# Performance work log

Hardware: AMD Instinct MI355X
Metric: run time of the kernel (lower is better)

Reference implementation:

```python
import jax, jax.numpy as jnp
import numpy as np


def setup_inputs() -> dict:
    key = jax.random.key(0)
    ks = jax.random.split(key, 12)
    B = 131072
    s = lambda fan_in: 1.0 / np.sqrt(fan_in)
    inp = {
        "x": jax.random.normal(ks[0], (B, 2, 13, 21), dtype=jnp.float32),
        # depthwise 3x3, groups=2, no bias: OIHW with O=2, I=1
        "dw_w": jax.random.uniform(ks[1], (2, 1, 3, 3), jnp.float32, -s(9), s(9)),
        # pointwise 1x1: 2 -> 5
        "pw_w": jax.random.uniform(ks[2], (5, 2, 1, 1), jnp.float32, -s(2), s(2)),
        "pw_b": jax.random.uniform(ks[3], (5,), jnp.float32, -s(2), s(2)),
        # conv 1x1: 5 -> 5
        "conv_w": jax.random.uniform(ks[4], (5, 5, 1, 1), jnp.float32, -s(5), s(5)),
        "conv_b": jax.random.uniform(ks[5], (5,), jnp.float32, -s(5), s(5)),
        # dense 90 -> 16 -> 16 -> 14 (torch Linear layout: [out, in])
        "w1": jax.random.uniform(ks[6], (16, 90), jnp.float32, -s(90), s(90)),
        "b1": jax.random.uniform(ks[7], (16,), jnp.float32, -s(90), s(90)),
        "w2": jax.random.uniform(ks[8], (16, 16), jnp.float32, -s(16), s(16)),
        "b2": jax.random.uniform(ks[9], (16,), jnp.float32, -s(16), s(16)),
        "w3": jax.random.uniform(ks[10], (14, 16), jnp.float32, -s(16), s(16)),
        "b3": jax.random.uniform(ks[11], (14,), jnp.float32, -s(16), s(16)),
    }
    return inp


def _conv(x, w, groups=1):
    return jax.lax.conv_general_dilated(
        x, w, window_strides=(1, 1), padding="VALID",
        dimension_numbers=("NCHW", "OIHW", "NCHW"),
        feature_group_count=groups)


def reference(x, dw_w, pw_w, pw_b, conv_w, conv_b, w1, b1, w2, b2, w3, b3):
    # depthwise-separable conv: depthwise 3x3 (groups=2, no bias) + pointwise 1x1
    h = _conv(x, dw_w, groups=2)                      # [B,2,11,19]
    h = _conv(h, pw_w) + pw_b[None, :, None, None]    # [B,5,11,19]
    h = jnp.tanh(h)
    h = _conv(h, conv_w) + conv_b[None, :, None, None]  # 1x1 conv 5->5
    h = jnp.tanh(h)
    # AvgPool2d(3): kernel=stride=3, no padding -> crop to 9x18, reshape-mean
    h = h[:, :, :9, :18]
    B = h.shape[0]
    h = h.reshape(B, 5, 3, 3, 6, 3).mean(axis=(3, 5))  # [B,5,3,6]
    h = jnp.tanh(h)
    h = h.reshape(B, 90)
    h = jnp.tanh(h @ w1.T + b1)
    h = jnp.tanh(h @ w2.T + b2)
    return h @ w3.T + b3                               # [B,14]
```

## Files before the change

### kernel.cpp

```cpp
#include <hip/hip_runtime.h>

typedef float f4v __attribute__((ext_vector_type(4), aligned(4)));
typedef float f2v __attribute__((ext_vector_type(2), aligned(4)));

__device__ __forceinline__ float fast_tanh(float x) {
  float t = x * 2.8853900817779268f;
  float e = __builtin_amdgcn_exp2f(t);
  float r = __builtin_amdgcn_rcpf(e + 1.0f);
  return 1.0f - 2.0f * r;
}

__global__ __launch_bounds__(256, 3) void smartpixel_kernel(
    const float* __restrict__ x, const float* __restrict__ dww,
    const float* __restrict__ pww, const float* __restrict__ pwb,
    const float* __restrict__ cvw, const float* __restrict__ cvb,
    const float* __restrict__ w1, const float* __restrict__ b1,
    const float* __restrict__ w2, const float* __restrict__ b2,
    const float* __restrict__ w3, const float* __restrict__ b3,
    float* __restrict__ out, int nsamp) {
  const int g = blockIdx.x * 256 + threadIdx.x;
  const int s = g >> 1;
  const int t = g & 1;
  if (s >= nsamp) return;
  const float* xb = x + (long)s * 546 + t * 9;

  float A0[12], A1[12], A2[12], A3[12];
  float B0[12], B1[12], B2[12], B3[12];

#define LDROW(S, R)                                                        \
  do {                                                                     \
    _Pragma("unroll") for (int kk = 0; kk < 3; ++kk) {                     \
      f4v va = *reinterpret_cast<const f4v*>(xb + (R) * 21 + 4 * kk);      \
      f4v vb = *reinterpret_cast<const f4v*>(xb + 273 + (R) * 21 + 4 * kk);\
      _Pragma("unroll") for (int l = 0; l < 4; ++l) {                      \
        A##S[4 * kk + l] = va[l];                                          \
        B##S[4 * kk + l] = vb[l];                                          \
      }                                                                    \
    }                                                                      \
  } while (0)

  float pool[5][3];
#pragma unroll
  for (int c = 0; c < 5; ++c)
#pragma unroll
    for (int pc = 0; pc < 3; ++pc) pool[c][pc] = 0.0f;

  float h1a[16];
#pragma unroll
  for (int o = 0; o < 16; ++o) h1a[o] = (t == 0) ? b1[o] : 0.0f;

  const float* w1t = w1 + 3 * t;

#define ROWBODY(SA, SB, SC)                                                   \
  do {                                                                        \
    _Pragma("unroll") for (int j = 0; j < 9; ++j) {                           \
      float d0 = A##SA[j] * dww[0] + A##SA[j + 1] * dww[1] + A##SA[j + 2] * dww[2]  \
               + A##SB[j] * dww[3] + A##SB[j + 1] * dww[4] + A##SB[j + 2] * dww[5]  \
               + A##SC[j] * dww[6] + A##SC[j + 1] * dww[7] + A##SC[j + 2] * dww[8]; \
      float d1 = B##SA[j] * dww[9]  + B##SA[j + 1] * dww[10] + B##SA[j + 2] * dww[11] \
               + B##SB[j] * dww[12] + B##SB[j + 1] * dww[13] + B##SB[j + 2] * dww[14] \
               + B##SC[j] * dww[15] + B##SC[j + 1] * dww[16] + B##SC[j + 2] * dww[17];\
      float aa0 = fast_tanh(pwb[0] + pww[0] * d0 + pww[1] * d1);              \
      float aa1 = fast_tanh(pwb[1] + pww[2] * d0 + pww[3] * d1);              \
      float aa2 = fast_tanh(pwb[2] + pww[4] * d0 + pww[5] * d1);              \
      float aa3 = fast_tanh(pwb[3] + pww[6] * d0 + pww[7] * d1);              \
      float aa4 = fast_tanh(pwb[4] + pww[8] * d0 + pww[9] * d1);              \
      _Pragma("unroll") for (int q = 0; q < 5; ++q) {                         \
        float acc = cvb[q] + cvw[5 * q] * aa0 + cvw[5 * q + 1] * aa1          \
                  + cvw[5 * q + 2] * aa2 + cvw[5 * q + 3] * aa3               \
                  + cvw[5 * q + 4] * aa4;                                     \
        pool[q][j / 3] += fast_tanh(acc);                                     \
      }                                                                       \
    }                                                                         \
  } while (0)

#define POOLFIN(RR)                                                           \
  do {                                                                        \
    _Pragma("unroll") for (int c = 0; c < 5; ++c) {                           \
      _Pragma("unroll") for (int pc = 0; pc < 3; ++pc) {                      \
        float pv = fast_tanh(pool[c][pc] * (1.0f / 9.0f));                    \
        pool[c][pc] = 0.0f;                                                   \
        _Pragma("unroll") for (int o = 0; o < 16; ++o) {                      \
          h1a[o] += pv * w1t[o * 90 + c * 18 + (RR) * 6 + pc];                \
        }                                                                     \
      }                                                                       \
    }                                                                         \
  } while (0)

  LDROW(0, 0); LDROW(1, 1); LDROW(2, 2);
  LDROW(3, 3);  ROWBODY(0, 1, 2);
  LDROW(0, 4);  ROWBODY(1, 2, 3);
  LDROW(1, 5);  ROWBODY(2, 3, 0); POOLFIN(0);
  LDROW(2, 6);  ROWBODY(3, 0, 1);
  LDROW(3, 7);  ROWBODY(0, 1, 2);
  LDROW(0, 8);  ROWBODY(1, 2, 3); POOLFIN(1);
  LDROW(1, 9);  ROWBODY(2, 3, 0);
  LDROW(2, 10); ROWBODY(3, 0, 1);
                ROWBODY(0, 1, 2); POOLFIN(2);

#pragma unroll
  for (int o = 0; o < 16; ++o) h1a[o] += __shfl_xor(h1a[o], 1, 64);

  float h1[16];
#pragma unroll
  for (int k = 0; k < 16; ++k) h1[k] = fast_tanh(h1a[k]);

  float h2[16];
#pragma unroll
  for (int o = 0; o < 16; ++o) {
    float acc = b2[o];
#pragma unroll
    for (int k = 0; k < 16; ++k) acc += h1[k] * w2[o * 16 + k];
    h2[o] = fast_tanh(acc);
  }

  const int ob = 7 * t;
  float ov[7];
#pragma unroll
  for (int oo = 0; oo < 7; ++oo) {
    float acc = b3[ob + oo];
#pragma unroll
    for (int k = 0; k < 16; ++k) acc += h2[k] * w3[(ob + oo) * 16 + k];
    ov[oo] = acc;
  }
  float* po = out + (long)s * 14 + ob;
  f4v v4; v4[0] = ov[0]; v4[1] = ov[1]; v4[2] = ov[2]; v4[3] = ov[3];
  *reinterpret_cast<f4v*>(po) = v4;
  f2v v2; v2[0] = ov[4]; v2[1] = ov[5];
  *reinterpret_cast<f2v*>(po + 4) = v2;
  po[6] = ov[6];
}

extern "C" void kernel_launch(void* const* d_in, const int* in_sizes, int n_in,
                              void* d_out, int out_size, void* d_ws, size_t ws_size,
                              hipStream_t stream) {
  const float* x      = (const float*)d_in[0];
  const float* dw_w   = (const float*)d_in[1];
  const float* pw_w   = (const float*)d_in[2];
  const float* pw_b   = (const float*)d_in[3];
  const float* conv_w = (const float*)d_in[4];
  const float* conv_b = (const float*)d_in[5];
  const float* w1     = (const float*)d_in[6];
  const float* b1     = (const float*)d_in[7];
  const float* w2     = (const float*)d_in[8];
  const float* b2     = (const float*)d_in[9];
  const float* w3     = (const float*)d_in[10];
  const float* b3     = (const float*)d_in[11];
  float* out = (float*)d_out;

  int nsamp = in_sizes[0] / 546;
  long nthreads = 2L * nsamp;
  int blocks = (int)((nthreads + 255) / 256);
  smartpixel_kernel<<<blocks, 256, 0, stream>>>(
      x, dw_w, pw_w, pw_b, conv_w, conv_b, w1, b1, w2, b2, w3, b3, out, nsamp);
}
```

Measured before the change: 127.3 us.

## Roll row pipeline into a two-iteration loop and hoist weights into scalars

Replaces the fully unrolled 11-row sweep with a two-iteration non-unrolled loop that keeps the 4-slot rolling row buffers, and hoists all conv weights into named scalar constants loaded once. Converts arrays to explicit scalars, vectorizes w1/w3 weight loads, splits the b1 bias as half per thread, and changes launch bounds to a waves-per-eu range of 2–3. The aim is smaller code size and less instruction-cache pressure with controlled register use. The cost is a loop back-edge, predicated pool-finish branches, and possibly lower occupancy if the compiler settles on 2 waves.

```diff
diff --git a/kernel.cpp b/kernel.cpp
--- a/kernel.cpp
+++ b/kernel.cpp
@@ -10,7 +10,9 @@
   return 1.0f - 2.0f * r;
 }
 
-__global__ __launch_bounds__(256, 3) void smartpixel_kernel(
+__global__ __launch_bounds__(256)
+__attribute__((amdgpu_waves_per_eu(2, 3)))
+void smartpixel_kernel(
     const float* __restrict__ x, const float* __restrict__ dww,
     const float* __restrict__ pww, const float* __restrict__ pwb,
     const float* __restrict__ cvw, const float* __restrict__ cvb,
@@ -24,111 +26,163 @@
   if (s >= nsamp) return;
   const float* xb = x + (long)s * 546 + t * 9;
 
-  float A0[12], A1[12], A2[12], A3[12];
-  float B0[12], B1[12], B2[12], B3[12];
-
-#define LDROW(S, R)                                                        \
-  do {                                                                     \
-    _Pragma("unroll") for (int kk = 0; kk < 3; ++kk) {                     \
-      f4v va = *reinterpret_cast<const f4v*>(xb + (R) * 21 + 4 * kk);      \
-      f4v vb = *reinterpret_cast<const f4v*>(xb + 273 + (R) * 21 + 4 * kk);\
-      _Pragma("unroll") for (int l = 0; l < 4; ++l) {                      \
-        A##S[4 * kk + l] = va[l];                                          \
-        B##S[4 * kk + l] = vb[l];                                          \
-      }                                                                    \
-    }                                                                      \
+  const float kd0 = dww[0], kd1 = dww[1], kd2 = dww[2], kd3 = dww[3], kd4 = dww[4],
+              kd5 = dww[5], kd6 = dww[6], kd7 = dww[7], kd8 = dww[8], kd9 = dww[9],
+              kd10 = dww[10], kd11 = dww[11], kd12 = dww[12], kd13 = dww[13],
+              kd14 = dww[14], kd15 = dww[15], kd16 = dww[16], kd17 = dww[17];
+  const float kp0 = pww[0], kp1 = pww[1], kp2 = pww[2], kp3 = pww[3], kp4 = pww[4],
+              kp5 = pww[5], kp6 = pww[6], kp7 = pww[7], kp8 = pww[8], kp9 = pww[9];
+  const float kb0 = pwb[0], kb1 = pwb[1], kb2 = pwb[2], kb3 = pwb[3], kb4 = pwb[4];
+  const float kc0 = cvw[0], kc1 = cvw[1], kc2 = cvw[2], kc3 = cvw[3], kc4 = cvw[4],
+              kc5 = cvw[5], kc6 = cvw[6], kc7 = cvw[7], kc8 = cvw[8], kc9 = cvw[9],
+              kc10 = cvw[10], kc11 = cvw[11], kc12 = cvw[12], kc13 = cvw[13],
+              kc14 = cvw[14], kc15 = cvw[15], kc16 = cvw[16], kc17 = cvw[17],
+              kc18 = cvw[18], kc19 = cvw[19], kc20 = cvw[20], kc21 = cvw[21],
+              kc22 = cvw[22], kc23 = cvw[23], kc24 = cvw[24];
+  const float kcb0 = cvb[0], kcb1 = cvb[1], kcb2 = cvb[2], kcb3 = cvb[3], kcb4 = cvb[4];
+
+#define DECLROW(P) float P##_0, P##_1, P##_2, P##_3, P##_4, P##_5, P##_6, P##_7, P##_8, P##_9, P##_10, P##_11;
+  DECLROW(A0) DECLROW(A1) DECLROW(A2) DECLROW(A3)
+  DECLROW(B0) DECLROW(B1) DECLROW(B2) DECLROW(B3)
+
+#define LDROW(S, BASE, R)                                                   \
+  do {                                                                      \
+    f4v va0 = *reinterpret_cast<const f4v*>((BASE) + (R) * 21 + 0);         \
+    f4v va1 = *reinterpret_cast<const f4v*>((BASE) + (R) * 21 + 4);         \
+    f4v va2 = *reinterpret_cast<const f4v*>((BASE) + (R) * 21 + 8);         \
+    f4v vb0 = *reinterpret_cast<const f4v*>((BASE) + 273 + (R) * 21 + 0);   \
+    f4v vb1 = *reinterpret_cast<const f4v*>((BASE) + 273 + (R) * 21 + 4);   \
+    f4v vb2 = *reinterpret_cast<const f4v*>((BASE) + 273 + (R) * 21 + 8);   \
+    A##S##_0 = va0[0]; A##S##_1 = va0[1]; A##S##_2 = va0[2]; A##S##_3 = va0[3]; \
+    A##S##_4 = va1[0]; A##S##_5 = va1[1]; A##S##_6 = va1[2]; A##S##_7 = va1[3]; \
+    A##S##_8 = va2[0]; A##S##_9 = va2[1]; A##S##_10 = va2[2]; A##S##_11 = va2[3]; \
+    B##S##_0 = vb0[0]; B##S##_1 = vb0[1]; B##S##_2 = vb0[2]; B##S##_3 = vb0[3]; \
+    B##S##_4 = vb1[0]; B##S##_5 = vb1[1]; B##S##_6 = vb1[2]; B##S##_7 = vb1[3]; \
+    B##S##_8 = vb2[0]; B##S##_9 = vb2[1]; B##S##_10 = vb2[2]; B##S##_11 = vb2[3]; \
   } while (0)
 
-  float pool[5][3];
-#pragma unroll
-  for (int c = 0; c < 5; ++c)
-#pragma unroll
-    for (int pc = 0; pc < 3; ++pc) pool[c][pc] = 0.0f;
-
-  float h1a[16];
-#pragma unroll
-  for (int o = 0; o < 16; ++o) h1a[o] = (t == 0) ? b1[o] : 0.0f;
+  float P0_0 = 0.f, P0_1 = 0.f, P0_2 = 0.f;
+  float P1_0 = 0.f, P1_1 = 0.f, P1_2 = 0.f;
+  float P2_0 = 0.f, P2_1 = 0.f, P2_2 = 0.f;
+  float P3_0 = 0.f, P3_1 = 0.f, P3_2 = 0.f;
+  float P4_0 = 0.f, P4_1 = 0.f, P4_2 = 0.f;
+  float H0 = 0.5f * b1[0], H1 = 0.5f * b1[1], H2 = 0.5f * b1[2], H3 = 0.5f * b1[3],
+        H4 = 0.5f * b1[4], H5 = 0.5f * b1[5], H6 = 0.5f * b1[6], H7 = 0.5f * b1[7],
+        H8 = 0.5f * b1[8], H9 = 0.5f * b1[9], H10 = 0.5f * b1[10], H11 = 0.5f * b1[11],
+        H12 = 0.5f * b1[12], H13 = 0.5f * b1[13], H14 = 0.5f * b1[14], H15 = 0.5f * b1[15];
+
+#define POS(SA, SB, SC, J0, J1, J2, G)                                        \
+  do {                                                                        \
+    float d0 = A##SA##_##J0 * kd0 + A##SA##_##J1 * kd1 + A##SA##_##J2 * kd2   \
+             + A##SB##_##J0 * kd3 + A##SB##_##J1 * kd4 + A##SB##_##J2 * kd5   \
+             + A##SC##_##J0 * kd6 + A##SC##_##J1 * kd7 + A##SC##_##J2 * kd8;  \
+    float d1 = B##SA##_##J0 * kd9 + B##SA##_##J1 * kd10 + B##SA##_##J2 * kd11 \
+             + B##SB##_##J0 * kd12 + B##SB##_##J1 * kd13 + B##SB##_##J2 * kd14\
+             + B##SC##_##J0 * kd15 + B##SC##_##J1 * kd16 + B##SC##_##J2 * kd17;\
+    float u0 = fast_tanh(kb0 + kp0 * d0 + kp1 * d1);                          \
+    float u1 = fast_tanh(kb1 + kp2 * d0 + kp3 * d1);                          \
+    float u2 = fast_tanh(kb2 + kp4 * d0 + kp5 * d1);                          \
+    float u3 = fast_tanh(kb3 + kp6 * d0 + kp7 * d1);                          \
+    float u4 = fast_tanh(kb4 + kp8 * d0 + kp9 * d1);                          \
+    P0_##G += fast_tanh(kcb0 + kc0 * u0 + kc1 * u1 + kc2 * u2 + kc3 * u3 + kc4 * u4);   \
+    P1_##G += fast_tanh(kcb1 + kc5 * u0 + kc6 * u1 + kc7 * u2 + kc8 * u3 + kc9 * u4);   \
+    P2_##G += fast_tanh(kcb2 + kc10 * u0 + kc11 * u1 + kc12 * u2 + kc13 * u3 + kc14 * u4); \
+    P3_##G += fast_tanh(kcb3 + kc15 * u0 + kc16 * u1 + kc17 * u2 + kc18 * u3 + kc19 * u4); \
+    P4_##G += fast_tanh(kcb4 + kc20 * u0 + kc21 * u1 + kc22 * u2 + kc23 * u3 + kc24 * u4); \
+  } while (0)
+
+#define ROWBODY(SA, SB, SC)                                                   \
+  POS(SA, SB, SC, 0, 1, 2, 0); POS(SA, SB, SC, 1, 2, 3, 0);                   \
+  POS(SA, SB, SC, 2, 3, 4, 0); POS(SA, SB, SC, 3, 4, 5, 1);                   \
+  POS(SA, SB, SC, 4, 5, 6, 1); POS(SA, SB, SC, 5, 6, 7, 1);                   \
+  POS(SA, SB, SC, 6, 7, 8, 2); POS(SA, SB, SC, 7, 8, 9, 2);                   \
+  POS(SA, SB, SC, 8, 9, 10, 2);
 
   const float* w1t = w1 + 3 * t;
 
-#define ROWBODY(SA, SB, SC)                                                   \
+#define ACC1(O, WP, p0_, p1_, p2_)                                            \
+  {                                                                           \
+    f2v wv = *reinterpret_cast<const f2v*>((WP) + (O) * 90);                  \
+    float ws = (WP)[(O) * 90 + 2];                                            \
+    H##O += p0_ * wv[0] + p1_ * wv[1] + p2_ * ws;                             \
+  }
+
+#define FCH(C, RR)                                                            \
   do {                                                                        \
-    _Pragma("unroll") for (int j = 0; j < 9; ++j) {                           \
-      float d0 = A##SA[j] * dww[0] + A##SA[j + 1] * dww[1] + A##SA[j + 2] * dww[2]  \
-               + A##SB[j] * dww[3] + A##SB[j + 1] * dww[4] + A##SB[j + 2] * dww[5]  \
-               + A##SC[j] * dww[6] + A##SC[j + 1] * dww[7] + A##SC[j + 2] * dww[8]; \
-      float d1 = B##SA[j] * dww[9]  + B##SA[j + 1] * dww[10] + B##SA[j + 2] * dww[11] \
-               + B##SB[j] * dww[12] + B##SB[j + 1] * dww[13] + B##SB[j + 2] * dww[14] \
-               + B##SC[j] * dww[15] + B##SC[j + 1] * dww[16] + B##SC[j + 2] * dww[17];\
-      float aa0 = fast_tanh(pwb[0] + pww[0] * d0 + pww[1] * d1);              \
-      float aa1 = fast_tanh(pwb[1] + pww[2] * d0 + pww[3] * d1);              \
-      float aa2 = fast_tanh(pwb[2] + pww[4] * d0 + pww[5] * d1);              \
-      float aa3 = fast_tanh(pwb[3] + pww[6] * d0 + pww[7] * d1);              \
-      float aa4 = fast_tanh(pwb[4] + pww[8] * d0 + pww[9] * d1);              \
-      _Pragma("unroll") for (int q = 0; q < 5; ++q) {                         \
-        float acc = cvb[q] + cvw[5 * q] * aa0 + cvw[5 * q + 1] * aa1          \
-                  + cvw[5 * q + 2] * aa2 + cvw[5 * q + 3] * aa3               \
-                  + cvw[5 * q + 4] * aa4;                                     \
-        pool[q][j / 3] += fast_tanh(acc);                                     \
-      }                                                                       \
-    }                                                                         \
+    float pv0 = fast_tanh(P##C##_0 * (1.0f / 9.0f)); P##C##_0 = 0.f;          \
+    float pv1 = fast_tanh(P##C##_1 * (1.0f / 9.0f)); P##C##_1 = 0.f;          \
+    float pv2 = fast_tanh(P##C##_2 * (1.0f / 9.0f)); P##C##_2 = 0.f;          \
+    const float* wp_ = w1t + (C) * 18 + (RR) * 6;                             \
+    ACC1(0, wp_, pv0, pv1, pv2) ACC1(1, wp_, pv0, pv1, pv2)                   \
+    ACC1(2, wp_, pv0, pv1, pv2) ACC1(3, wp_, pv0, pv1, pv2)                   \
+    ACC1(4, wp_, pv0, pv1, pv2) ACC1(5, wp_, pv0, pv1, pv2)                   \
+    ACC1(6, wp_, pv0, pv1, pv2) ACC1(7, wp_, pv0, pv1, pv2)                   \
+    ACC1(8, wp_, pv0, pv1, pv2) ACC1(9, wp_, pv0, pv1, pv2)                   \
+    ACC1(10, wp_, pv0, pv1, pv2) ACC1(11, wp_, pv0, pv1, pv2)                 \
+    ACC1(12, wp_, pv0, pv1, pv2) ACC1(13, wp_, pv0, pv1, pv2)                 \
+    ACC1(14, wp_, pv0, pv1, pv2) ACC1(15, wp_, pv0, pv1, pv2)                 \
   } while (0)
 
-#define POOLFIN(RR)                                                           \
-  do {                                                                        \
-    _Pragma("unroll") for (int c = 0; c < 5; ++c) {                           \
-      _Pragma("unroll") for (int pc = 0; pc < 3; ++pc) {                      \
-        float pv = fast_tanh(pool[c][pc] * (1.0f / 9.0f));                    \
-        pool[c][pc] = 0.0f;                                                   \
-        _Pragma("unroll") for (int o = 0; o < 16; ++o) {                      \
-          h1a[o] += pv * w1t[o * 90 + c * 18 + (RR) * 6 + pc];                \
-        }                                                                     \
-      }                                                                       \
-    }                                                                         \
-  } while (0)
-
-  LDROW(0, 0); LDROW(1, 1); LDROW(2, 2);
-  LDROW(3, 3);  ROWBODY(0, 1, 2);
-  LDROW(0, 4);  ROWBODY(1, 2, 3);
-  LDROW(1, 5);  ROWBODY(2, 3, 0); POOLFIN(0);
-  LDROW(2, 6);  ROWBODY(3, 0, 1);
-  LDROW(3, 7);  ROWBODY(0, 1, 2);
-  LDROW(0, 8);  ROWBODY(1, 2, 3); POOLFIN(1);
-  LDROW(1, 9);  ROWBODY(2, 3, 0);
-  LDROW(2, 10); ROWBODY(3, 0, 1);
-                ROWBODY(0, 1, 2); POOLFIN(2);
-
-#pragma unroll
-  for (int o = 0; o < 16; ++o) h1a[o] += __shfl_xor(h1a[o], 1, 64);
-
-  float h1[16];
-#pragma unroll
-  for (int k = 0; k < 16; ++k) h1[k] = fast_tanh(h1a[k]);
-
-  float h2[16];
-#pragma unroll
-  for (int o = 0; o < 16; ++o) {
-    float acc = b2[o];
-#pragma unroll
-    for (int k = 0; k < 16; ++k) acc += h1[k] * w2[o * 16 + k];
-    h2[o] = fast_tanh(acc);
+#define POOLFIN(RR) FCH(0, RR); FCH(1, RR); FCH(2, RR); FCH(3, RR); FCH(4, RR);
+
+  LDROW(0, xb, 0); LDROW(1, xb, 1); LDROW(2, xb, 2);
+
+#pragma unroll 1
+  for (int ig = 0; ig < 2; ++ig) {
+    const float* xr = xb + (long)ig * 84;
+    LDROW(3, xr, 3);
+    ROWBODY(0, 1, 2);
+    LDROW(0, xr, 4);
+    ROWBODY(1, 2, 3);
+    if (ig == 1) { POOLFIN(1); }
+    LDROW(1, xr, 5);
+    ROWBODY(2, 3, 0);
+    if (ig == 0) { POOLFIN(0); }
+    LDROW(2, xr, 6);
+    ROWBODY(3, 0, 1);
   }
+  ROWBODY(0, 1, 2);
+  POOLFIN(2);
+
+#define COMB(O) H##O += __shfl_xor(H##O, 1, 64); H##O = fast_tanh(H##O);
+  COMB(0) COMB(1) COMB(2) COMB(3) COMB(4) COMB(5) COMB(6) COMB(7)
+  COMB(8) COMB(9) COMB(10) COMB(11) COMB(12) COMB(13) COMB(14) COMB(15)
+
+#define FC2(O)                                                                \
+  float q##O = fast_tanh(b2[(O)]                                              \
+      + H0 * w2[(O) * 16 + 0] + H1 * w2[(O) * 16 + 1] + H2 * w2[(O) * 16 + 2] \
+      + H3 * w2[(O) * 16 + 3] + H4 * w2[(O) * 16 + 4] + H5 * w2[(O) * 16 + 5] \
+      + H6 * w2[(O) * 16 + 6] + H7 * w2[(O) * 16 + 7] + H8 * w2[(O) * 16 + 8] \
+      + H9 * w2[(O) * 16 + 9] + H10 * w2[(O) * 16 + 10]                       \
+      + H11 * w2[(O) * 16 + 11] + H12 * w2[(O) * 16 + 12]                     \
+      + H13 * w2[(O) * 16 + 13] + H14 * w2[(O) * 16 + 14]                     \
+      + H15 * w2[(O) * 16 + 15]);
+  FC2(0) FC2(1) FC2(2) FC2(3) FC2(4) FC2(5) FC2(6) FC2(7)
+  FC2(8) FC2(9) FC2(10) FC2(11) FC2(12) FC2(13) FC2(14) FC2(15)
 
   const int ob = 7 * t;
-  float ov[7];
-#pragma unroll
-  for (int oo = 0; oo < 7; ++oo) {
-    float acc = b3[ob + oo];
-#pragma unroll
-    for (int k = 0; k < 16; ++k) acc += h2[k] * w3[(ob + oo) * 16 + k];
-    ov[oo] = acc;
+  const float* w3t = w3 + ob * 16;
+#define OUT1(OO)                                                              \
+  float o##OO;                                                                \
+  {                                                                           \
+    f4v wa = *reinterpret_cast<const f4v*>(w3t + (OO) * 16 + 0);              \
+    f4v wb = *reinterpret_cast<const f4v*>(w3t + (OO) * 16 + 4);              \
+    f4v wc = *reinterpret_cast<const f4v*>(w3t + (OO) * 16 + 8);              \
+    f4v wd = *reinterpret_cast<const f4v*>(w3t + (OO) * 16 + 12);             \
+    o##OO = b3[ob + (OO)]                                                     \
+        + q0 * wa[0] + q1 * wa[1] + q2 * wa[2] + q3 * wa[3]                   \
+        + q4 * wb[0] + q5 * wb[1] + q6 * wb[2] + q7 * wb[3]                   \
+        + q8 * wc[0] + q9 * wc[1] + q10 * wc[2] + q11 * wc[3]                 \
+        + q12 * wd[0] + q13 * wd[1] + q14 * wd[2] + q15 * wd[3];              \
   }
+  OUT1(0) OUT1(1) OUT1(2) OUT1(3) OUT1(4) OUT1(5) OUT1(6)
+
   float* po = out + (long)s * 14 + ob;
-  f4v v4; v4[0] = ov[0]; v4[1] = ov[1]; v4[2] = ov[2]; v4[3] = ov[3];
-  *reinterpret_cast<f4v*>(po) = v4;
-  f2v v2; v2[0] = ov[4]; v2[1] = ov[5];
-  *reinterpret_cast<f2v*>(po + 4) = v2;
-  po[6] = ov[6];
+  f4v s4; s4[0] = o0; s4[1] = o1; s4[2] = o2; s4[3] = o3;
+  *reinterpret_cast<f4v*>(po) = s4;
+  f2v s2; s2[0] = o4; s2[1] = o5;
+  *reinterpret_cast<f2v*>(po + 4) = s2;
+  po[6] = o6;
 }
 
 extern "C" void kernel_launch(void* const* d_in, const int* in_sizes, int n_in,
```

Result: slower. 206.6 us (+62.2%).

## Split each sample across four threads with shared pooling via shuffles

Applied to the files above, without the earlier changes.

Each sample is now handled by four lanes instead of two. Each lane covers a narrower column strip, and the pooling windows that straddle two lanes are combined with a shuffle. The row loop is rolled (unroll 1) with a 3-slot row buffer, and weights are hoisted into scalars, which raises occupancy (launch bounds 4) and cuts registers per thread. In exchange, the MLP tail (FC2) is computed redundantly in all four lanes, there are more shuffles, and lanes 1 and 3 compute unequal work, which causes divergence.

```diff
diff --git a/kernel.cpp b/kernel.cpp
--- a/kernel.cpp
+++ b/kernel.cpp
@@ -10,7 +10,7 @@
   return 1.0f - 2.0f * r;
 }
 
-__global__ __launch_bounds__(256, 3) void smartpixel_kernel(
+__global__ __launch_bounds__(256, 4) void smartpixel_kernel(
     const float* __restrict__ x, const float* __restrict__ dww,
     const float* __restrict__ pww, const float* __restrict__ pwb,
     const float* __restrict__ cvw, const float* __restrict__ cvb,
@@ -19,116 +19,180 @@
     const float* __restrict__ w3, const float* __restrict__ b3,
     float* __restrict__ out, int nsamp) {
   const int g = blockIdx.x * 256 + threadIdx.x;
-  const int s = g >> 1;
-  const int t = g & 1;
+  const int s = g >> 2;
+  const int t = g & 3;
   if (s >= nsamp) return;
-  const float* xb = x + (long)s * 546 + t * 9;
-
-  float A0[12], A1[12], A2[12], A3[12];
-  float B0[12], B1[12], B2[12], B3[12];
-
-#define LDROW(S, R)                                                        \
-  do {                                                                     \
-    _Pragma("unroll") for (int kk = 0; kk < 3; ++kk) {                     \
-      f4v va = *reinterpret_cast<const f4v*>(xb + (R) * 21 + 4 * kk);      \
-      f4v vb = *reinterpret_cast<const f4v*>(xb + 273 + (R) * 21 + 4 * kk);\
-      _Pragma("unroll") for (int l = 0; l < 4; ++l) {                      \
-        A##S[4 * kk + l] = va[l];                                          \
-        B##S[4 * kk + l] = vb[l];                                          \
-      }                                                                    \
-    }                                                                      \
-  } while (0)
-
-  float pool[5][3];
-#pragma unroll
-  for (int c = 0; c < 5; ++c)
-#pragma unroll
-    for (int pc = 0; pc < 3; ++pc) pool[c][pc] = 0.0f;
-
-  float h1a[16];
-#pragma unroll
-  for (int o = 0; o < 16; ++o) h1a[o] = (t == 0) ? b1[o] : 0.0f;
-
-  const float* w1t = w1 + 3 * t;
-
-#define ROWBODY(SA, SB, SC)                                                   \
-  do {                                                                        \
-    _Pragma("unroll") for (int j = 0; j < 9; ++j) {                           \
-      float d0 = A##SA[j] * dww[0] + A##SA[j + 1] * dww[1] + A##SA[j + 2] * dww[2]  \
-               + A##SB[j] * dww[3] + A##SB[j + 1] * dww[4] + A##SB[j + 2] * dww[5]  \
-               + A##SC[j] * dww[6] + A##SC[j + 1] * dww[7] + A##SC[j + 2] * dww[8]; \
-      float d1 = B##SA[j] * dww[9]  + B##SA[j + 1] * dww[10] + B##SA[j + 2] * dww[11] \
-               + B##SB[j] * dww[12] + B##SB[j + 1] * dww[13] + B##SB[j + 2] * dww[14] \
-               + B##SC[j] * dww[15] + B##SC[j + 1] * dww[16] + B##SC[j + 2] * dww[17];\
-      float aa0 = fast_tanh(pwb[0] + pww[0] * d0 + pww[1] * d1);              \
-      float aa1 = fast_tanh(pwb[1] + pww[2] * d0 + pww[3] * d1);              \
-      float aa2 = fast_tanh(pwb[2] + pww[4] * d0 + pww[5] * d1);              \
-      float aa3 = fast_tanh(pwb[3] + pww[6] * d0 + pww[7] * d1);              \
-      float aa4 = fast_tanh(pwb[4] + pww[8] * d0 + pww[9] * d1);              \
-      _Pragma("unroll") for (int q = 0; q < 5; ++q) {                         \
-        float acc = cvb[q] + cvw[5 * q] * aa0 + cvw[5 * q + 1] * aa1          \
-                  + cvw[5 * q + 2] * aa2 + cvw[5 * q + 3] * aa3               \
-                  + cvw[5 * q + 4] * aa4;                                     \
-        pool[q][j / 3] += fast_tanh(acc);                                     \
-      }                                                                       \
-    }                                                                         \
-  } while (0)
-
-#define POOLFIN(RR)                                                           \
-  do {                                                                        \
-    _Pragma("unroll") for (int c = 0; c < 5; ++c) {                           \
-      _Pragma("unroll") for (int pc = 0; pc < 3; ++pc) {                      \
-        float pv = fast_tanh(pool[c][pc] * (1.0f / 9.0f));                    \
-        pool[c][pc] = 0.0f;                                                   \
-        _Pragma("unroll") for (int o = 0; o < 16; ++o) {                      \
-          h1a[o] += pv * w1t[o * 90 + c * 18 + (RR) * 6 + pc];                \
-        }                                                                     \
-      }                                                                       \
-    }                                                                         \
-  } while (0)
-
-  LDROW(0, 0); LDROW(1, 1); LDROW(2, 2);
-  LDROW(3, 3);  ROWBODY(0, 1, 2);
-  LDROW(0, 4);  ROWBODY(1, 2, 3);
-  LDROW(1, 5);  ROWBODY(2, 3, 0); POOLFIN(0);
-  LDROW(2, 6);  ROWBODY(3, 0, 1);
-  LDROW(3, 7);  ROWBODY(0, 1, 2);
-  LDROW(0, 8);  ROWBODY(1, 2, 3); POOLFIN(1);
-  LDROW(1, 9);  ROWBODY(2, 3, 0);
-  LDROW(2, 10); ROWBODY(3, 0, 1);
-                ROWBODY(0, 1, 2); POOLFIN(2);
-
-#pragma unroll
-  for (int o = 0; o < 16; ++o) h1a[o] += __shfl_xor(h1a[o], 1, 64);
-
-  float h1[16];
-#pragma unroll
-  for (int k = 0; k < 16; ++k) h1[k] = fast_tanh(h1a[k]);
-
-  float h2[16];
-#pragma unroll
-  for (int o = 0; o < 16; ++o) {
-    float acc = b2[o];
-#pragma unroll
-    for (int k = 0; k < 16; ++k) acc += h1[k] * w2[o * 16 + k];
-    h2[o] = fast_tanh(acc);
-  }
-
-  const int ob = 7 * t;
-  float ov[7];
-#pragma unroll
-  for (int oo = 0; oo < 7; ++oo) {
-    float acc = b3[ob + oo];
-#pragma unroll
-    for (int k = 0; k < 16; ++k) acc += h2[k] * w3[(ob + oo) * 16 + k];
-    ov[oo] = acc;
-  }
-  float* po = out + (long)s * 14 + ob;
-  f4v v4; v4[0] = ov[0]; v4[1] = ov[1]; v4[2] = ov[2]; v4[3] = ov[3];
-  *reinterpret_cast<f4v*>(po) = v4;
-  f2v v2; v2[0] = ov[4]; v2[1] = ov[5];
-  *reinterpret_cast<f2v*>(po + 4) = v2;
-  po[6] = ov[6];
+
+  const int cb = (0x0D090500u >> (8 * t)) & 0xFF;
+  const float* xb = x + (long)s * 546 + cb;
+  const bool tOdd = (t & 1) != 0;
+  const bool isT1 = (t == 1), isT3 = (t == 3);
+  const int hT = t >> 1;
+
+  const float kd0 = dww[0], kd1 = dww[1], kd2 = dww[2], kd3 = dww[3], kd4 = dww[4],
+              kd5 = dww[5], kd6 = dww[6], kd7 = dww[7], kd8 = dww[8], kd9 = dww[9],
+              kd10 = dww[10], kd11 = dww[11], kd12 = dww[12], kd13 = dww[13],
+              kd14 = dww[14], kd15 = dww[15], kd16 = dww[16], kd17 = dww[17];
+  const float kp0 = pww[0], kp1 = pww[1], kp2 = pww[2], kp3 = pww[3], kp4 = pww[4],
+              kp5 = pww[5], kp6 = pww[6], kp7 = pww[7], kp8 = pww[8], kp9 = pww[9];
+  const float kb0 = pwb[0], kb1 = pwb[1], kb2 = pwb[2], kb3 = pwb[3], kb4 = pwb[4];
+  const float kc0 = cvw[0], kc1 = cvw[1], kc2 = cvw[2], kc3 = cvw[3], kc4 = cvw[4],
+              kc5 = cvw[5], kc6 = cvw[6], kc7 = cvw[7], kc8 = cvw[8], kc9 = cvw[9],
+              kc10 = cvw[10], kc11 = cvw[11], kc12 = cvw[12], kc13 = cvw[13],
+              kc14 = cvw[14], kc15 = cvw[15], kc16 = cvw[16], kc17 = cvw[17],
+              kc18 = cvw[18], kc19 = cvw[19], kc20 = cvw[20], kc21 = cvw[21],
+              kc22 = cvw[22], kc23 = cvw[23], kc24 = cvw[24];
+  const float kcb0 = cvb[0], kcb1 = cvb[1], kcb2 = cvb[2], kcb3 = cvb[3], kcb4 = cvb[4];
+
+#define DECLSLOT(S)                                                          \
+  float XA##S##_0, XA##S##_1, XA##S##_2, XA##S##_3, XA##S##_4, XA##S##_5,    \
+      XA##S##_6, XA##S##_7, XB##S##_0, XB##S##_1, XB##S##_2, XB##S##_3,      \
+      XB##S##_4, XB##S##_5, XB##S##_6, XB##S##_7;
+  DECLSLOT(0) DECLSLOT(1) DECLSLOT(2)
+
+#define LDROW(S, PTR)                                                        \
+  do {                                                                       \
+    const float* p_ = (PTR);                                                 \
+    f4v a0_ = *reinterpret_cast<const f4v*>(p_);                             \
+    f4v a1_ = *reinterpret_cast<const f4v*>(p_ + 4);                         \
+    f4v c0_ = *reinterpret_cast<const f4v*>(p_ + 273);                       \
+    f4v c1_ = *reinterpret_cast<const f4v*>(p_ + 277);                       \
+    XA##S##_0 = a0_[0]; XA##S##_1 = a0_[1]; XA##S##_2 = a0_[2];              \
+    XA##S##_3 = a0_[3]; XA##S##_4 = a1_[0]; XA##S##_5 = a1_[1];              \
+    XA##S##_6 = a1_[2]; XA##S##_7 = a1_[3];                                  \
+    XB##S##_0 = c0_[0]; XB##S##_1 = c0_[1]; XB##S##_2 = c0_[2];              \
+    XB##S##_3 = c0_[3]; XB##S##_4 = c1_[0]; XB##S##_5 = c1_[1];              \
+    XB##S##_6 = c1_[2]; XB##S##_7 = c1_[3];                                  \
+  } while (0)
+
+  float P0_0 = 0.f, P0_1 = 0.f, P0_2 = 0.f, P0_3 = 0.f, P0_4 = 0.f;
+  float P1_0 = 0.f, P1_1 = 0.f, P1_2 = 0.f, P1_3 = 0.f, P1_4 = 0.f;
+  float P2_0 = 0.f, P2_1 = 0.f, P2_2 = 0.f, P2_3 = 0.f, P2_4 = 0.f;
+  float P3_0 = 0.f, P3_1 = 0.f, P3_2 = 0.f, P3_3 = 0.f, P3_4 = 0.f;
+  float P4_0 = 0.f, P4_1 = 0.f, P4_2 = 0.f, P4_3 = 0.f, P4_4 = 0.f;
+
+  float H0 = 0.f, H1 = 0.f, H2 = 0.f, H3 = 0.f, H4 = 0.f, H5 = 0.f, H6 = 0.f,
+        H7 = 0.f, H8 = 0.f, H9 = 0.f, H10 = 0.f, H11 = 0.f, H12 = 0.f,
+        H13 = 0.f, H14 = 0.f, H15 = 0.f;
+
+#define POS(SA, SB, SC, J0, J1, J2, PP)                                      \
+  do {                                                                       \
+    float d0 = XA##SA##_##J0 * kd0 + XA##SA##_##J1 * kd1 + XA##SA##_##J2 * kd2 \
+             + XA##SB##_##J0 * kd3 + XA##SB##_##J1 * kd4 + XA##SB##_##J2 * kd5 \
+             + XA##SC##_##J0 * kd6 + XA##SC##_##J1 * kd7 + XA##SC##_##J2 * kd8; \
+    float d1 = XB##SA##_##J0 * kd9 + XB##SA##_##J1 * kd10 + XB##SA##_##J2 * kd11 \
+             + XB##SB##_##J0 * kd12 + XB##SB##_##J1 * kd13 + XB##SB##_##J2 * kd14 \
+             + XB##SC##_##J0 * kd15 + XB##SC##_##J1 * kd16 + XB##SC##_##J2 * kd17; \
+    float u0 = fast_tanh(kb0 + kp0 * d0 + kp1 * d1);                         \
+    float u1 = fast_tanh(kb1 + kp2 * d0 + kp3 * d1);                         \
+    float u2 = fast_tanh(kb2 + kp4 * d0 + kp5 * d1);                         \
+    float u3 = fast_tanh(kb3 + kp6 * d0 + kp7 * d1);                         \
+    float u4 = fast_tanh(kb4 + kp8 * d0 + kp9 * d1);                         \
+    P0_##PP += fast_tanh(kcb0 + kc0 * u0 + kc1 * u1 + kc2 * u2 + kc3 * u3 + kc4 * u4);   \
+    P1_##PP += fast_tanh(kcb1 + kc5 * u0 + kc6 * u1 + kc7 * u2 + kc8 * u3 + kc9 * u4);   \
+    P2_##PP += fast_tanh(kcb2 + kc10 * u0 + kc11 * u1 + kc12 * u2 + kc13 * u3 + kc14 * u4); \
+    P3_##PP += fast_tanh(kcb3 + kc15 * u0 + kc16 * u1 + kc17 * u2 + kc18 * u3 + kc19 * u4); \
+    P4_##PP += fast_tanh(kcb4 + kc20 * u0 + kc21 * u1 + kc22 * u2 + kc23 * u3 + kc24 * u4); \
+  } while (0)
+
+#define ROWBODY(SA, SB, SC)                                                  \
+  do {                                                                       \
+    if (!isT3) POS(SA, SB, SC, 0, 1, 2, 0);                                  \
+    POS(SA, SB, SC, 1, 2, 3, 1);                                             \
+    POS(SA, SB, SC, 2, 3, 4, 2);                                             \
+    POS(SA, SB, SC, 3, 4, 5, 3);                                             \
+    if (!isT1) POS(SA, SB, SC, 4, 5, 6, 4);                                  \
+  } while (0)
+
+#define ACCH(O)                                                              \
+  {                                                                          \
+    f2v wv = *reinterpret_cast<const f2v*>(wb_ + (O) * 90);                  \
+    H##O += clo * wv[0] + chi * wv[1];                                       \
+  }
+#define FCH1(C)                                                              \
+  do {                                                                       \
+    float sA = P##C##_0 + P##C##_1 + P##C##_2;                               \
+    float sMe = P##C##_3 + P##C##_4;                                         \
+    float sMo = isT3 ? P##C##_1 : P##C##_0;                                  \
+    float myMid = tOdd ? sMo : sMe;                                          \
+    float sB = P##C##_2 + P##C##_3 + (isT3 ? P##C##_4 : P##C##_1);           \
+    float midFull = myMid + __shfl_xor(myMid, 1, 64);                        \
+    float pvA = fast_tanh(sA * (1.0f / 9.0f));                               \
+    float sHi = tOdd ? sB : midFull;                                         \
+    float chi = fast_tanh(sHi * (1.0f / 9.0f));                              \
+    float clo = tOdd ? 0.0f : pvA;                                           \
+    const float* wb_ = w1 + (C) * 18 + rr6 + hT * 3 + (tOdd ? 1 : 0);        \
+    ACCH(0) ACCH(1) ACCH(2) ACCH(3) ACCH(4) ACCH(5) ACCH(6) ACCH(7)          \
+    ACCH(8) ACCH(9) ACCH(10) ACCH(11) ACCH(12) ACCH(13) ACCH(14) ACCH(15)    \
+    P##C##_0 = 0.f; P##C##_1 = 0.f; P##C##_2 = 0.f; P##C##_3 = 0.f;          \
+    P##C##_4 = 0.f;                                                          \
+  } while (0)
+
+  LDROW(0, xb);
+  LDROW(1, xb + 21);
+
+#pragma unroll 1
+  for (int rg = 0; rg < 3; ++rg) {
+    const float* xr = xb + rg * 63;
+    const int rr6 = rg * 6;
+    LDROW(2, xr + 42);
+    ROWBODY(0, 1, 2);
+    LDROW(0, xr + 63);
+    ROWBODY(1, 2, 0);
+    LDROW(1, xr + 84);
+    ROWBODY(2, 0, 1);
+    FCH1(0); FCH1(1); FCH1(2); FCH1(3); FCH1(4);
+  }
+
+#define RED(O)                                                               \
+  H##O += __shfl_xor(H##O, 1, 64);                                           \
+  H##O += __shfl_xor(H##O, 2, 64);                                           \
+  H##O = fast_tanh(H##O + b1[O]);
+  RED(0) RED(1) RED(2) RED(3) RED(4) RED(5) RED(6) RED(7)
+  RED(8) RED(9) RED(10) RED(11) RED(12) RED(13) RED(14) RED(15)
+
+#define FC2(O)                                                               \
+  float q##O = fast_tanh(b2[(O)]                                             \
+      + H0 * w2[(O) * 16 + 0] + H1 * w2[(O) * 16 + 1] + H2 * w2[(O) * 16 + 2]\
+      + H3 * w2[(O) * 16 + 3] + H4 * w2[(O) * 16 + 4] + H5 * w2[(O) * 16 + 5]\
+      + H6 * w2[(O) * 16 + 6] + H7 * w2[(O) * 16 + 7] + H8 * w2[(O) * 16 + 8]\
+      + H9 * w2[(O) * 16 + 9] + H10 * w2[(O) * 16 + 10]                      \
+      + H11 * w2[(O) * 16 + 11] + H12 * w2[(O) * 16 + 12]                    \
+      + H13 * w2[(O) * 16 + 13] + H14 * w2[(O) * 16 + 14]                    \
+      + H15 * w2[(O) * 16 + 15]);
+  FC2(0) FC2(1) FC2(2) FC2(3) FC2(4) FC2(5) FC2(6) FC2(7)
+  FC2(8) FC2(9) FC2(10) FC2(11) FC2(12) FC2(13) FC2(14) FC2(15)
+
+  const int base = 4 * t - (hT & (t & 1));
+  const float* w3t = w3 + base * 16;
+#define DOT3(OO, ROFF)                                                       \
+  float o##OO;                                                               \
+  {                                                                          \
+    f4v wa = *reinterpret_cast<const f4v*>(w3t + (ROFF) + 0);                \
+    f4v wb = *reinterpret_cast<const f4v*>(w3t + (ROFF) + 4);                \
+    f4v wc = *reinterpret_cast<const f4v*>(w3t + (ROFF) + 8);                \
+    f4v wd = *reinterpret_cast<const f4v*>(w3t + (ROFF) + 12);               \
+    o##OO = b3[base + (OO)]                                                  \
+        + q0 * wa[0] + q1 * wa[1] + q2 * wa[2] + q3 * wa[3]                  \
+        + q4 * wb[0] + q5 * wb[1] + q6 * wb[2] + q7 * wb[3]                  \
+        + q8 * wc[0] + q9 * wc[1] + q10 * wc[2] + q11 * wc[3]                \
+        + q12 * wd[0] + q13 * wd[1] + q14 * wd[2] + q15 * wd[3];             \
+  }
+  DOT3(0, 0) DOT3(1, 16) DOT3(2, 32)
+  float* po = out + (long)s * 14 + base;
+  if (t < 2) {
+    DOT3(3, 48)
+    f4v v; v[0] = o0; v[1] = o1; v[2] = o2; v[3] = o3;
+    *reinterpret_cast<f4v*>(po) = v;
+  } else if (t == 2) {
+    f2v v; v[0] = o0; v[1] = o1;
+    *reinterpret_cast<f2v*>(po) = v;
+    po[2] = o2;
+  } else {
+    po[0] = o0;
+    f2v v; v[0] = o1; v[1] = o2;
+    *reinterpret_cast<f2v*>(po + 1) = v;
+  }
 }
 
 extern "C" void kernel_launch(void* const* d_in, const int* in_sizes, int n_in,
@@ -149,7 +213,7 @@
   float* out = (float*)d_out;
 
   int nsamp = in_sizes[0] / 546;
-  long nthreads = 2L * nsamp;
+  long nthreads = 4L * nsamp;
   int blocks = (int)((nthreads + 255) / 256);
   smartpixel_kernel<<<blocks, 256, 0, stream>>>(
       x, dw_w, pw_w, pw_b, conv_w, conv_b, w1, b1, w2, b2, w3, b3, out, nsamp);
```

New measurement: 136.5 us. +7.2%, slower.
